# Kernel tuning notes

Hardware: AMD Instinct MI355X
Metric: run time of the kernel (lower is better)

## Reference

```python
import jax, jax.numpy as jnp
import numpy as np

# --- static config (from init_kwargs) ---
B = 256        # num graphs
NPG = 128      # nodes per graph
EPG = 512      # edges per graph
DIN = 128      # dim_node
D = 256        # dim_hidden
RATIO = 0.5    # causal_ratio
N_RES = int(RATIO * EPG)
BN_EPS = 1e-5


def setup_inputs() -> dict:
    key = jax.random.key(0)
    ks = jax.random.split(key, 24)
    N = B * NPG
    x = jax.random.normal(ks[0], (N, DIN), jnp.float32)
    # edges confined within each graph, contiguous per graph (graph-sorted)
    src = jax.random.randint(ks[1], (B, EPG), 0, NPG)
    dst = jax.random.randint(ks[2], (B, EPG), 0, NPG)
    off = (jnp.arange(B, dtype=jnp.int32) * NPG)[:, None]
    edge_index = jnp.stack([(src + off).reshape(-1), (dst + off).reshape(-1)], 0).astype(jnp.int32)
    batch = jnp.repeat(jnp.arange(B, dtype=jnp.int32), NPG)

    s = 0.05
    def rn(k, shape):
        return jax.random.normal(k, shape, jnp.float32) * s
    p = dict(
        x=x, edge_index=edge_index, batch=batch,
        vemb=rn(ks[3], (1, D)),
        # conv1 GIN mlp: Linear(DIN,2D) -> BN -> ReLU -> Linear(2D,D)
        W1a=rn(ks[4], (DIN, 2 * D)), b1a=jnp.zeros((2 * D,)),
        g1a=jnp.ones((2 * D,)), be1a=jnp.zeros((2 * D,)),
        W1b=rn(ks[5], (2 * D, D)), b1b=jnp.zeros((D,)),
        g1=jnp.ones((D,)), be1=jnp.zeros((D,)),          # outer batch_norm1
        # conv2 GIN mlp
        W2a=rn(ks[6], (D, 2 * D)), b2a=jnp.zeros((2 * D,)),
        g2a=jnp.ones((2 * D,)), be2a=jnp.zeros((2 * D,)),
        W2b=rn(ks[7], (2 * D, D)), b2b=jnp.zeros((D,)),
        g2=jnp.ones((D,)), be2=jnp.zeros((D,)),          # outer batch_norm2
        # edge scorer: Linear(2D, 1)
        Wl=rn(ks[8], (2 * D, 1)), bl=jnp.zeros((1,)),
    )
    return p


def _bn(h, g, b):
    mu = h.mean(0)
    var = jnp.mean((h - mu) ** 2, 0)
    return (h - mu) * jax.lax.rsqrt(var + BN_EPS) * g + b


def reference(x, edge_index, batch, vemb,
              W1a, b1a, g1a, be1a, W1b, b1b, g1, be1,
              W2a, b2a, g2a, be2a, W2b, b2b, g2, be2,
              Wl, bl):
    N = x.shape[0]
    row, col = edge_index[0], edge_index[1]

    def gin(h, Wa, ba, ga, bta, Wb, bb):
        # GINConv, eps=0: mlp(h + sum_{j->i} h_j), aggregate src feats at dst
        agg = jax.ops.segment_sum(h[row], col, num_segments=N)
        z = (h + agg) @ Wa + ba
        z = jax.nn.relu(_bn(z, ga, bta))
        return z @ Wb + bb

    # layer 1: conv1 -> bn -> relu (dropout_rate = 0)
    post = jax.nn.relu(_bn(gin(x, W1a, b1a, g1a, be1a, W1b, b1b), g1, be1))
    # virtual node gather (embedding of index 0, one per graph)
    vfeat = jnp.broadcast_to(vemb[0], (B, D))
    post = post + vfeat[batch]
    # layer 2 (last): conv2 -> bn, no relu
    xn = _bn(gin(post, W2a, b2a, g2a, be2a, W2b, b2b), g2, be2)

    # edge scoring
    erep = jnp.concatenate([xn[row], xn[col]], axis=-1)          # [E, 2D]
    pred = (erep @ Wl + bl.astype(erep.dtype)).reshape(-1)       # [E]

    # per-graph top-k split (equal EPG edges per graph)
    pw = pred.reshape(B, EPG)
    order = jnp.argsort(-pw, axis=1)
    idx_r, idx_d = order[:, :N_RES], order[:, N_RES:]
    causal_w = jnp.take_along_axis(pw, idx_r, 1).reshape(-1)
    conf_w = -jnp.take_along_axis(pw, idx_d, 1).reshape(-1)
    ei = edge_index.reshape(2, B, EPG)
    causal_ei = jnp.take_along_axis(ei, jnp.broadcast_to(idx_r[None], (2, B, N_RES)), axis=2).reshape(2, -1)
    conf_ei = jnp.take_along_axis(ei, jnp.broadcast_to(idx_d[None], (2, B, EPG - N_RES)), axis=2).reshape(2, -1)
    return (causal_ei, causal_w, conf_ei, conf_w, pred)
```

## Files before the change

kernel.cpp:

```cpp
#include <hip/hip_runtime.h>

#define BGR   256
#define NPG   128
#define EPG   512
#define DIN   128
#define DD    256
#define DD2   512
#define NTOT  (BGR * NPG)
#define ETOT  (BGR * EPG)
#define NRES  (EPG / 2)
#define NCHUNK 256
#define MP    136

#define OFF_CEI  0
#define OFF_CW   (2 * BGR * NRES)
#define OFF_FEI  (OFF_CW + BGR * NRES)
#define OFF_FW   (OFF_FEI + 2 * BGR * NRES)
#define OFF_PRED (OFF_FW + BGR * NRES)

typedef unsigned short ushortt;
typedef __attribute__((ext_vector_type(4))) unsigned short us4;
typedef __attribute__((ext_vector_type(8))) unsigned short us8;
typedef __attribute__((ext_vector_type(8))) short short8;
typedef __attribute__((ext_vector_type(4))) float f32x4;

__device__ __forceinline__ ushortt f2bf(float f) {
    unsigned int u = __float_as_uint(f);
    unsigned int r = (u + 0x7fffu + ((u >> 16) & 1u)) >> 16;
    return (ushortt)r;
}
__device__ __forceinline__ float bf2f(ushortt u) {
    return __uint_as_float(((unsigned int)u) << 16);
}

__device__ __forceinline__ void g2lds16(const void* g, void* l) {
    __builtin_amdgcn_global_load_lds(
        (const __attribute__((address_space(1))) unsigned int*)g,
        (__attribute__((address_space(3))) unsigned int*)l, 16, 0, 0);
}

__global__ __launch_bounds__(256) void convert_all(const float* __restrict__ W1a,
                                                   const float* __restrict__ W1b,
                                                   const float* __restrict__ W2a,
                                                   const float* __restrict__ W2b,
                                                   ushortt* __restrict__ Wt1a,
                                                   ushortt* __restrict__ Wt1b,
                                                   ushortt* __restrict__ Wt2a,
                                                   ushortt* __restrict__ Wt2b) {
    const int idx = blockIdx.x * 256 + threadIdx.x;
    if (idx < 65536) {
        const int k = idx >> 9, n = idx & 511;
        Wt1a[n * DIN + k] = f2bf(W1a[idx]);
    } else if (idx < 196608) {
        const int i = idx - 65536;
        const int k = i >> 8, n = i & 255;
        Wt1b[n * DD2 + k] = f2bf(W1b[i]);
    } else if (idx < 327680) {
        const int i = idx - 196608;
        const int k = i >> 9, n = i & 511;
        Wt2a[n * DD + k] = f2bf(W2a[i]);
    } else if (idx < 458752) {
        const int i = idx - 327680;
        const int k = i >> 8, n = i & 255;
        Wt2b[n * DD2 + k] = f2bf(W2b[i]);
    }
}

__global__ __launch_bounds__(256) void build_adj(const int* __restrict__ ei,
                                                 ushortt* __restrict__ Madj) {
    __shared__ int cnt[NPG * NPG];
    const int b = blockIdx.x, t = threadIdx.x;
    for (int i = t; i < NPG * NPG; i += 256) cnt[i] = 0;
    __syncthreads();
    for (int e = t; e < EPG; e += 256) {
        const int src = ei[b * EPG + e] - b * NPG;
        const int dst = ei[ETOT + b * EPG + e] - b * NPG;
        atomicAdd(&cnt[dst * NPG + src], 1);
    }
    __syncthreads();
#pragma unroll
    for (int k = 0; k < 8; ++k) {
        const int i0 = (t + k * 256) * 8;
        us8 o;
#pragma unroll
        for (int e = 0; e < 8; ++e) {
            const int i = i0 + e;
            const int v = cnt[i] + (((i >> 7) == (i & 127)) ? 1 : 0);
            o[e] = f2bf((float)v);
        }
        *(us8*)&Madj[(size_t)b * NPG * NPG + i0] = o;
    }
}

__global__ __launch_bounds__(256) void agg1_mm(const float* __restrict__ x,
                                               const ushortt* __restrict__ Madj,
                                               ushortt* __restrict__ s1) {
    __shared__ ushortt Ms[NPG * MP];
    __shared__ ushortt XT[DIN * MP];
    const int b = blockIdx.x, t = threadIdx.x;
    const int wave = t >> 6, lane = t & 63;
    const int qd = lane >> 4, r = lane & 15;
    const ushortt* Mg = Madj + (size_t)b * NPG * NPG;
#pragma unroll
    for (int k = 0; k < 8; ++k) {
        const int ch = t + k * 256;
        const int m = ch >> 4, sc = (ch & 15) * 8;
        *(us8*)&Ms[m * MP + sc] = *(const us8*)&Mg[m * NPG + sc];
    }
#pragma unroll 4
    for (int it = 0; it < 64; ++it) {
        const int s = it * 2 + (t >> 7);
        const int c = t & 127;
        XT[c * MP + s] = f2bf(x[(size_t)(b * NPG + s) * DIN + c]);
    }
    __syncthreads();
    const int wm = (wave >> 1) * 64, wn = (wave & 1) * 64;
    f32x4 acc[4][4] = {};
#pragma unroll
    for (int ks = 0; ks < 4; ++ks) {
        const int k0 = ks * 32 + qd * 8;
        short8 af[4], bfr[4];
#pragma unroll
        for (int i = 0; i < 4; ++i)
            af[i] = *(const short8*)&Ms[(wm + i * 16 + r) * MP + k0];
#pragma unroll
        for (int j = 0; j < 4; ++j)
            bfr[j] = *(const short8*)&XT[(wn + j * 16 + r) * MP + k0];
#pragma unroll
        for (int i = 0; i < 4; ++i)
#pragma unroll
            for (int j = 0; j < 4; ++j)
                acc[i][j] = __builtin_amdgcn_mfma_f32_16x16x32_bf16(af[i], bfr[j], acc[i][j], 0, 0, 0);
    }
    __syncthreads();
    ushortt* Cs = Ms;
#pragma unroll
    for (int j = 0; j < 4; ++j) {
        const int coll = wn + j * 16 + r;
#pragma unroll
        for (int i = 0; i < 4; ++i)
#pragma unroll
            for (int tt = 0; tt < 4; ++tt)
                Cs[(wm + i * 16 + qd * 4 + tt) * DIN + coll] = f2bf(acc[i][j][tt]);
    }
    __syncthreads();
#pragma unroll
    for (int k = 0; k < 8; ++k) {
        const int ch = t + k * 256;
        const int row = ch >> 4, colc = (ch & 15) * 8;
        *(us8*)&s1[(size_t)(b * NPG + row) * DIN + colc] = *(const us8*)&Cs[row * DIN + colc];
    }
}

__global__ __launch_bounds__(256) void agg2_mm(const ushortt* __restrict__ h,
                                               const float* __restrict__ scale,
                                               const float* __restrict__ shift,
                                               const float* __restrict__ vemb,
                                               const ushortt* __restrict__ Madj,
                                               ushortt* __restrict__ s2) {
    __shared__ ushortt Ms[NPG * MP];
    __shared__ ushortt PT[NPG * MP];
    const int nb = blockIdx.x, b = blockIdx.y, t = threadIdx.x;
    const int wave = t >> 6, lane = t & 63;
    const int qd = lane >> 4, r = lane & 15;
    const ushortt* Mg = Madj + (size_t)b * NPG * NPG;
#pragma unroll
    for (int k = 0; k < 8; ++k) {
        const int ch = t + k * 256;
        const int m = ch >> 4, sc = (ch & 15) * 8;
        *(us8*)&Ms[m * MP + sc] = *(const us8*)&Mg[m * NPG + sc];
    }
    const int cl = t & 127;
    const int c = nb * 128 + cl;
    const float scv = scale[c], shv = shift[c], vev = vemb[c];
#pragma unroll 4
    for (int it = 0; it < 64; ++it) {
        const int s = it * 2 + (t >> 7);
        float v = fmaf(bf2f(h[(size_t)(b * NPG + s) * DD + c]), scv, shv);
        PT[cl * MP + s] = f2bf(fmaxf(v, 0.0f) + vev);
    }
    __syncthreads();
    const int wm = (wave >> 1) * 64, wn = (wave & 1) * 64;
    f32x4 acc[4][4] = {};
#pragma unroll
    for (int ks = 0; ks < 4; ++ks) {
        const int k0 = ks * 32 + qd * 8;
        short8 af[4], bfr[4];
#pragma unroll
        for (int i = 0; i < 4; ++i)
            af[i] = *(const short8*)&Ms[(wm + i * 16 + r) * MP + k0];
#pragma unroll
        for (int j = 0; j < 4; ++j)
            bfr[j] = *(const short8*)&PT[(wn + j * 16 + r) * MP + k0];
#pragma unroll
        for (int i = 0; i < 4; ++i)
#pragma unroll
            for (int j = 0; j < 4; ++j)
                acc[i][j] = __builtin_amdgcn_mfma_f32_16x16x32_bf16(af[i], bfr[j], acc[i][j], 0, 0, 0);
    }
    __syncthreads();
    ushortt* Cs = Ms;
#pragma unroll
    for (int j = 0; j < 4; ++j) {
        const int coll = wn + j * 16 + r;
#pragma unroll
        for (int i = 0; i < 4; ++i)
#pragma unroll
            for (int tt = 0; tt < 4; ++tt)
                Cs[(wm + i * 16 + qd * 4 + tt) * 128 + coll] = f2bf(acc[i][j][tt]);
    }
    __syncthreads();
#pragma unroll
    for (int k = 0; k < 8; ++k) {
        const int ch = t + k * 256;
        const int row = ch >> 4, colc = (ch & 15) * 8;
        *(us8*)&s2[(size_t)(b * NPG + row) * DD + nb * 128 + colc] =
            *(const us8*)&Cs[row * 128 + colc];
    }
}

#define BM 128
#define BN 128
#define BK 32
__global__ __launch_bounds__(256) void gemm_mfma(const ushortt* __restrict__ A,
                                                 const ushortt* __restrict__ Wt,
                                                 const float* __restrict__ bias,
                                                 ushortt* __restrict__ C,
                                                 float* __restrict__ psum,
                                                 float* __restrict__ psumsq,
                                                 int M, int N, int K) {
    __shared__ ushortt As[BM * BK];
    __shared__ ushortt Bs[BN * BK];
    __shared__ ushortt Cs[BM * BN];
    __shared__ float redS[2][BN];
    __shared__ float redQ[2][BN];
    const int tid  = threadIdx.x;
    const int wave = tid >> 6;
    const int lane = tid & 63;
    const int qd = lane >> 4;
    const int r  = lane & 15;
    const int wm = (wave >> 1) * 64;
    const int wn = (wave & 1) * 64;
    const int m0 = blockIdx.y * BM;
    const int n0 = blockIdx.x * BN;

    f32x4 acc[4][4] = {};

    for (int k0 = 0; k0 < K; k0 += BK) {
#pragma unroll
        for (int s = 0; s < 2; ++s) {
            const int o   = wave * 128 + s * 64 + lane;
            const int row = o >> 2;
            const int cg  = o & 3;
            g2lds16(A  + (size_t)(m0 + row) * K + k0 + cg * 8,
                    &As[(size_t)(wave * 128 + s * 64) * 8]);
            g2lds16(Wt + (size_t)(n0 + row) * K + k0 + cg * 8,
                    &Bs[(size_t)(wave * 128 + s * 64) * 8]);
        }
        __syncthreads();
        short8 af[4], bfr[4];
#pragma unroll
        for (int i = 0; i < 4; ++i)
            af[i] = *(const short8*)&As[(wm + i * 16 + r) * BK + qd * 8];
#pragma unroll
        for (int j = 0; j < 4; ++j)
            bfr[j] = *(const short8*)&Bs[(wn + j * 16 + r) * BK + qd * 8];
#pragma unroll
        for (int i = 0; i < 4; ++i)
#pragma unroll
            for (int j = 0; j < 4; ++j)
                acc[i][j] = __builtin_amdgcn_mfma_f32_16x16x32_bf16(af[i], bfr[j], acc[i][j], 0, 0, 0);
        __syncthreads();
    }

#pragma unroll
    for (int j = 0; j < 4; ++j) {
        const int coll = wn + j * 16 + r;
        const float bv = bias[n0 + coll];
        float s = 0.0f, q = 0.0f;
#pragma unroll
        for (int i = 0; i < 4; ++i) {
#pragma unroll
            for (int t = 0; t < 4; ++t) {
                const float v = acc[i][j][t] + bv;
                Cs[(wm + i * 16 + qd * 4 + t) * BN + coll] = f2bf(v);
                s += v;
                q = fmaf(v, v, q);
            }
        }
        s += __shfl_xor(s, 16); s += __shfl_xor(s, 32);
        q += __shfl_xor(q, 16); q += __shfl_xor(q, 32);
        if (qd == 0) {
            redS[wave >> 1][coll] = s;
            redQ[wave >> 1][coll] = q;
        }
    }
    __syncthreads();
    if (tid < BN) {
        psum[(size_t)blockIdx.y * N + n0 + tid]   = redS[0][tid] + redS[1][tid];
        psumsq[(size_t)blockIdx.y * N + n0 + tid] = redQ[0][tid] + redQ[1][tid];
    }
#pragma unroll
    for (int s8 = 0; s8 < 8; ++s8) {
        const int c    = tid + 256 * s8;
        const int row  = c >> 4;
        const int colc = (c & 15) * 8;
        const us8 v = *(const us8*)&Cs[row * BN + colc];
        *(us8*)&C[(size_t)(m0 + row) * N + n0 + colc] = v;
    }
}

__global__ __launch_bounds__(256) void bn_finalize(const float* __restrict__ psum,
                                                   const float* __restrict__ psumsq,
                                                   const float* __restrict__ g,
                                                   const float* __restrict__ be,
                                                   int ncols,
                                                   float* __restrict__ scale,
                                                   float* __restrict__ shift) {
    const int c = blockIdx.x * 256 + threadIdx.x;
    double s = 0.0, s2 = 0.0;
    for (int k = 0; k < NCHUNK; ++k) {
        s += (double)psum[(size_t)k * ncols + c];
        s2 += (double)psumsq[(size_t)k * ncols + c];
    }
    const double mean = s / (double)NTOT;
    const double var = s2 / (double)NTOT - mean * mean;
    const double rs = 1.0 / sqrt(var + 1e-5);
    const float sc = (float)((double)g[c] * rs);
    scale[c] = sc;
    shift[c] = (float)((double)be[c] - mean * (double)sc);
}

__global__ __launch_bounds__(256) void bn_apply_vec(const ushortt* __restrict__ z,
                                                    const float* __restrict__ scale,
                                                    const float* __restrict__ shift,
                                                    ushortt* __restrict__ outp,
                                                    int ncolmask) {
    const size_t gi = (size_t)blockIdx.x * 256 + threadIdx.x;
    const size_t base = gi * 8;
    const int c0 = (int)(base & (size_t)ncolmask);
    const us8 z8 = *(const us8*)&z[base];
    us8 o;
#pragma unroll
    for (int e = 0; e < 8; ++e) {
        float v = fmaf(bf2f(z8[e]), scale[c0 + e], shift[c0 + e]);
        v = fmaxf(v, 0.0f);
        o[e] = f2bf(v);
    }
    *(us8*)&outp[base] = o;
}

__global__ __launch_bounds__(256) void node_dots_bn(const ushortt* __restrict__ h2,
                                                    const float* __restrict__ scale,
                                                    const float* __restrict__ shift,
                                                    const float* __restrict__ Wl,
                                                    float* __restrict__ pa,
                                                    float* __restrict__ pb) {
    const int wave = threadIdx.x >> 6;
    const int lane = threadIdx.x & 63;
    const int node = blockIdx.x * 4 + wave;
    const us4 z4 = *(const us4*)&h2[(size_t)node * DD + lane * 4];
    const float4 sc = *(const float4*)&scale[lane * 4];
    const float4 sh = *(const float4*)&shift[lane * 4];
    const float4 w0 = *(const float4*)&Wl[lane * 4];
    const float4 w1 = *(const float4*)&Wl[DD + lane * 4];
    const float x0 = fmaf(bf2f(z4.x), sc.x, sh.x);
    const float x1 = fmaf(bf2f(z4.y), sc.y, sh.y);
    const float x2 = fmaf(bf2f(z4.z), sc.z, sh.z);
    const float x3 = fmaf(bf2f(z4.w), sc.w, sh.w);
    float sa = x0 * w0.x + x1 * w0.y + x2 * w0.z + x3 * w0.w;
    float sb = x0 * w1.x + x1 * w1.y + x2 * w1.z + x3 * w1.w;
#pragma unroll
    for (int off = 32; off >= 1; off >>= 1) {
        sa += __shfl_down(sa, off);
        sb += __shfl_down(sb, off);
    }
    if (lane == 0) {
        pa[node] = sa;
        pb[node] = sb;
    }
}

__global__ __launch_bounds__(EPG) void sort_write(const float* __restrict__ pa,
                                                  const float* __restrict__ pb,
                                                  const float* __restrict__ bl,
                                                  const int* __restrict__ ei,
                                                  float* __restrict__ out) {
    __shared__ float pw[EPG];
    __shared__ int ord[EPG];
    const int b = blockIdx.x;
    const int t = threadIdx.x;
    const int rg = ei[b * EPG + t];
    const int cg = ei[ETOT + b * EPG + t];
    const float v = pa[rg] + pb[cg] + bl[0];
    pw[t] = v;
    out[OFF_PRED + b * EPG + t] = v;
    __syncthreads();
    int rank = 0;
#pragma unroll 8
    for (int k = 0; k < EPG; ++k) {
        const float u = pw[k];
        rank += (u > v) || (u == v && k < t);
    }
    ord[rank] = t;
    __syncthreads();
    const int j = ord[t];
    const float wv = pw[j];
    const float e0 = (float)ei[b * EPG + j];
    const float e1 = (float)ei[ETOT + b * EPG + j];
    if (t < NRES) {
        out[OFF_CEI + b * NRES + t] = e0;
        out[OFF_CEI + BGR * NRES + b * NRES + t] = e1;
        out[OFF_CW + b * NRES + t] = wv;
    } else {
        const int p = t - NRES;
        out[OFF_FEI + b * NRES + p] = e0;
        out[OFF_FEI + BGR * NRES + b * NRES + p] = e1;
        out[OFF_FW + b * NRES + p] = -wv;
    }
}

extern "C" void kernel_launch(void* const* d_in, const int* in_sizes, int n_in,
                              void* d_out, int out_size, void* d_ws, size_t ws_size,
                              hipStream_t stream) {
    (void)in_sizes; (void)n_in; (void)out_size; (void)ws_size;
    const float* x    = (const float*)d_in[0];
    const int*   ei   = (const int*)d_in[1];
    const float* vemb = (const float*)d_in[3];
    const float* W1a  = (const float*)d_in[4];
    const float* b1a  = (const float*)d_in[5];
    const float* g1a  = (const float*)d_in[6];
    const float* be1a = (const float*)d_in[7];
    const float* W1b  = (const float*)d_in[8];
    const float* b1b  = (const float*)d_in[9];
    const float* g1   = (const float*)d_in[10];
    const float* be1  = (const float*)d_in[11];
    const float* W2a  = (const float*)d_in[12];
    const float* b2a  = (const float*)d_in[13];
    const float* g2a  = (const float*)d_in[14];
    const float* be2a = (const float*)d_in[15];
    const float* W2b  = (const float*)d_in[16];
    const float* b2b  = (const float*)d_in[17];
    const float* g2   = (const float*)d_in[18];
    const float* be2  = (const float*)d_in[19];
    const float* Wl   = (const float*)d_in[20];
    const float* bl   = (const float*)d_in[21];
    float* out = (float*)d_out;

    char* wp = (char*)d_ws;
    auto alloc = [&](size_t bytes) -> char* {
        char* r = wp;
        wp += (bytes + 255) & ~(size_t)255;
        return r;
    };
    ushortt* zb    = (ushortt*)alloc((size_t)NTOT * 512 * 2);
    ushortt* bufC  = (ushortt*)alloc((size_t)NTOT * 512 * 2);
    ushortt* bufD  = (ushortt*)alloc((size_t)NTOT * 256 * 2);
    ushortt* bufS1 = (ushortt*)alloc((size_t)NTOT * 128 * 2);
    ushortt* Madj  = (ushortt*)alloc((size_t)BGR * NPG * NPG * 2);
    ushortt* Wt1a  = (ushortt*)alloc((size_t)DIN * DD2 * 2);
    ushortt* Wt1b  = (ushortt*)alloc((size_t)DD2 * DD * 2);
    ushortt* Wt2a  = (ushortt*)alloc((size_t)DD * DD2 * 2);
    ushortt* Wt2b  = (ushortt*)alloc((size_t)DD2 * DD * 2);
    float*   psum   = (float*)alloc((size_t)NCHUNK * 512 * 4);
    float*   psumsq = (float*)alloc((size_t)NCHUNK * 512 * 4);
    float*   scale  = (float*)alloc(512 * 4);
    float*   shift  = (float*)alloc(512 * 4);
    float*   pa     = (float*)alloc((size_t)NTOT * 4);
    float*   pb     = (float*)alloc((size_t)NTOT * 4);

    convert_all<<<1792, 256, 0, stream>>>(W1a, W1b, W2a, W2b, Wt1a, Wt1b, Wt2a, Wt2b);

    build_adj<<<BGR, 256, 0, stream>>>(ei, Madj);

    agg1_mm<<<BGR, 256, 0, stream>>>(x, Madj, bufS1);

    gemm_mfma<<<dim3(DD2 / BN, NTOT / BM), 256, 0, stream>>>(bufS1, Wt1a, b1a, zb, psum, psumsq, NTOT, DD2, DIN);
    bn_finalize<<<2, 256, 0, stream>>>(psum, psumsq, g1a, be1a, DD2, scale, shift);
    bn_apply_vec<<<(NTOT * DD2) / 2048, 256, 0, stream>>>(zb, scale, shift, bufC, DD2 - 1);

    gemm_mfma<<<dim3(DD / BN, NTOT / BM), 256, 0, stream>>>(bufC, Wt1b, b1b, zb, psum, psumsq, NTOT, DD, DD2);
    bn_finalize<<<1, 256, 0, stream>>>(psum, psumsq, g1, be1, DD, scale, shift);

    agg2_mm<<<dim3(2, BGR), 256, 0, stream>>>(zb, scale, shift, vemb, Madj, bufD);

    gemm_mfma<<<dim3(DD2 / BN, NTOT / BM), 256, 0, stream>>>(bufD, Wt2a, b2a, zb, psum, psumsq, NTOT, DD2, DD);
    bn_finalize<<<2, 256, 0, stream>>>(psum, psumsq, g2a, be2a, DD2, scale, shift);
    bn_apply_vec<<<(NTOT * DD2) / 2048, 256, 0, stream>>>(zb, scale, shift, bufC, DD2 - 1);

    gemm_mfma<<<dim3(DD / BN, NTOT / BM), 256, 0, stream>>>(bufC, Wt2b, b2b, zb, psum, psumsq, NTOT, DD, DD2);
    bn_finalize<<<1, 256, 0, stream>>>(psum, psumsq, g2, be2, DD, scale, shift);

    node_dots_bn<<<NTOT / 4, 256, 0, stream>>>(zb, scale, shift, Wl, pa, pb);

    sort_write<<<BGR, EPG, 0, stream>>>(pa, pb, bl, ei, out);
}
```

Measured before the change: 344.7 us.

## Fuse BN-apply into GEMM prologue and BN-finalize into consumers, merge prep kernels

Folds the BatchNorm scale/shift and ReLU into the A-tile load of the second GEMM in each GIN MLP, which removes the separate bn_apply pass over the 512-wide intermediate. The BN finalize for the 256-wide outputs moves into agg2_mm and into a new sort_mega kernel, which also absorbs the per-node dot products. Weight conversion and adjacency building are merged into one launch. Together these cut kernel launches and full-tensor round trips, but every consuming block now redundantly reduces the 256 partial-sum chunks in double precision.

```diff
diff --git a/kernel.cpp b/kernel.cpp
--- a/kernel.cpp
+++ b/kernel.cpp
@@ -39,37 +39,39 @@
         (__attribute__((address_space(3))) unsigned int*)l, 16, 0, 0);
 }
 
-__global__ __launch_bounds__(256) void convert_all(const float* __restrict__ W1a,
-                                                   const float* __restrict__ W1b,
-                                                   const float* __restrict__ W2a,
-                                                   const float* __restrict__ W2b,
-                                                   ushortt* __restrict__ Wt1a,
-                                                   ushortt* __restrict__ Wt1b,
-                                                   ushortt* __restrict__ Wt2a,
-                                                   ushortt* __restrict__ Wt2b) {
-    const int idx = blockIdx.x * 256 + threadIdx.x;
-    if (idx < 65536) {
-        const int k = idx >> 9, n = idx & 511;
-        Wt1a[n * DIN + k] = f2bf(W1a[idx]);
-    } else if (idx < 196608) {
-        const int i = idx - 65536;
-        const int k = i >> 8, n = i & 255;
-        Wt1b[n * DD2 + k] = f2bf(W1b[i]);
-    } else if (idx < 327680) {
-        const int i = idx - 196608;
-        const int k = i >> 9, n = i & 511;
-        Wt2a[n * DD + k] = f2bf(W2a[i]);
-    } else if (idx < 458752) {
-        const int i = idx - 327680;
-        const int k = i >> 8, n = i & 255;
-        Wt2b[n * DD2 + k] = f2bf(W2b[i]);
-    }
-}
-
-__global__ __launch_bounds__(256) void build_adj(const int* __restrict__ ei,
-                                                 ushortt* __restrict__ Madj) {
+__global__ __launch_bounds__(256) void prep(const float* __restrict__ W1a,
+                                            const float* __restrict__ W1b,
+                                            const float* __restrict__ W2a,
+                                            const float* __restrict__ W2b,
+                                            const int* __restrict__ ei,
+                                            ushortt* __restrict__ Wt1a,
+                                            ushortt* __restrict__ Wt1b,
+                                            ushortt* __restrict__ Wt2a,
+                                            ushortt* __restrict__ Wt2b,
+                                            ushortt* __restrict__ Madj) {
     __shared__ int cnt[NPG * NPG];
-    const int b = blockIdx.x, t = threadIdx.x;
+    const int t = threadIdx.x;
+    if (blockIdx.x < 1792) {
+        const int idx = blockIdx.x * 256 + t;
+        if (idx < 65536) {
+            const int k = idx >> 9, n = idx & 511;
+            Wt1a[n * DIN + k] = f2bf(W1a[idx]);
+        } else if (idx < 196608) {
+            const int i = idx - 65536;
+            const int k = i >> 8, n = i & 255;
+            Wt1b[n * DD2 + k] = f2bf(W1b[i]);
+        } else if (idx < 327680) {
+            const int i = idx - 196608;
+            const int k = i >> 9, n = i & 511;
+            Wt2a[n * DD + k] = f2bf(W2a[i]);
+        } else if (idx < 458752) {
+            const int i = idx - 327680;
+            const int k = i >> 8, n = i & 255;
+            Wt2b[n * DD2 + k] = f2bf(W2b[i]);
+        }
+        return;
+    }
+    const int b = blockIdx.x - 1792;
     for (int i = t; i < NPG * NPG; i += 256) cnt[i] = 0;
     __syncthreads();
     for (int e = t; e < EPG; e += 256) {
@@ -153,13 +155,18 @@
 }
 
 __global__ __launch_bounds__(256) void agg2_mm(const ushortt* __restrict__ h,
-                                               const float* __restrict__ scale,
-                                               const float* __restrict__ shift,
+                                               const float* __restrict__ psum,
+                                               const float* __restrict__ psumsq,
+                                               const float* __restrict__ g,
+                                               const float* __restrict__ be,
                                                const float* __restrict__ vemb,
                                                const ushortt* __restrict__ Madj,
                                                ushortt* __restrict__ s2) {
     __shared__ ushortt Ms[NPG * MP];
     __shared__ ushortt PT[NPG * MP];
+    __shared__ double redS[2][128];
+    __shared__ double redQ[2][128];
+    __shared__ float scs[128], shs[128];
     const int nb = blockIdx.x, b = blockIdx.y, t = threadIdx.x;
     const int wave = t >> 6, lane = t & 63;
     const int qd = lane >> 4, r = lane & 15;
@@ -170,9 +177,34 @@
         const int m = ch >> 4, sc = (ch & 15) * 8;
         *(us8*)&Ms[m * MP + sc] = *(const us8*)&Mg[m * NPG + sc];
     }
+    {
+        const int cl = t & 127, half = t >> 7;
+        const int c = nb * 128 + cl;
+        double s = 0.0, q = 0.0;
+#pragma unroll 4
+        for (int k = half * 128; k < half * 128 + 128; ++k) {
+            s += (double)psum[(size_t)k * DD + c];
+            q += (double)psumsq[(size_t)k * DD + c];
+        }
+        redS[half][cl] = s;
+        redQ[half][cl] = q;
+    }
+    __syncthreads();
+    if (t < 128) {
+        const int c = nb * 128 + t;
+        const double s = redS[0][t] + redS[1][t];
+        const double q = redQ[0][t] + redQ[1][t];
+        const double mean = s / (double)NTOT;
+        const double var = q / (double)NTOT - mean * mean;
+        const double rs = 1.0 / sqrt(var + 1e-5);
+        const float sc = (float)((double)g[c] * rs);
+        scs[t] = sc;
+        shs[t] = (float)((double)be[c] - mean * (double)sc);
+    }
+    __syncthreads();
     const int cl = t & 127;
     const int c = nb * 128 + cl;
-    const float scv = scale[c], shv = shift[c], vev = vemb[c];
+    const float scv = scs[cl], shv = shs[cl], vev = vemb[c];
 #pragma unroll 4
     for (int it = 0; it < 64; ++it) {
         const int s = it * 2 + (t >> 7);
@@ -310,6 +342,122 @@
     }
 }
 
+__global__ __launch_bounds__(256) void gemm_mfma_bn(const ushortt* __restrict__ A,
+                                                    const ushortt* __restrict__ Wt,
+                                                    const float* __restrict__ scale,
+                                                    const float* __restrict__ shift,
+                                                    const float* __restrict__ bias,
+                                                    ushortt* __restrict__ C,
+                                                    float* __restrict__ psum,
+                                                    float* __restrict__ psumsq,
+                                                    int M, int N, int K) {
+    __shared__ ushortt As[BM * BK];
+    __shared__ ushortt Bs[BN * BK];
+    __shared__ ushortt Cs[BM * BN];
+    __shared__ float redS[2][BN];
+    __shared__ float redQ[2][BN];
+    __shared__ float scs[DD2], shs[DD2];
+    const int tid  = threadIdx.x;
+    const int wave = tid >> 6;
+    const int lane = tid & 63;
+    const int qd = lane >> 4;
+    const int r  = lane & 15;
+    const int wm = (wave >> 1) * 64;
+    const int wn = (wave & 1) * 64;
+    const int m0 = blockIdx.y * BM;
+    const int n0 = blockIdx.x * BN;
+
+    for (int i = tid; i < K; i += 256) {
+        scs[i] = scale[i];
+        shs[i] = shift[i];
+    }
+    __syncthreads();
+
+    f32x4 acc[4][4] = {};
+
+    for (int k0 = 0; k0 < K; k0 += BK) {
+#pragma unroll
+        for (int s = 0; s < 2; ++s) {
+            const int o   = wave * 128 + s * 64 + lane;
+            const int row = o >> 2;
+            const int cg  = o & 3;
+            g2lds16(Wt + (size_t)(n0 + row) * K + k0 + cg * 8,
+                    &Bs[(size_t)(wave * 128 + s * 64) * 8]);
+        }
+#pragma unroll
+        for (int s = 0; s < 2; ++s) {
+            const int o   = wave * 128 + s * 64 + lane;
+            const int row = o >> 2;
+            const int cg  = o & 3;
+            const us8 a8 = *(const us8*)&A[(size_t)(m0 + row) * K + k0 + cg * 8];
+            const float4 s4a = *(const float4*)&scs[k0 + cg * 8];
+            const float4 s4b = *(const float4*)&scs[k0 + cg * 8 + 4];
+            const float4 h4a = *(const float4*)&shs[k0 + cg * 8];
+            const float4 h4b = *(const float4*)&shs[k0 + cg * 8 + 4];
+            us8 t8;
+            t8[0] = f2bf(fmaxf(fmaf(bf2f(a8[0]), s4a.x, h4a.x), 0.0f));
+            t8[1] = f2bf(fmaxf(fmaf(bf2f(a8[1]), s4a.y, h4a.y), 0.0f));
+            t8[2] = f2bf(fmaxf(fmaf(bf2f(a8[2]), s4a.z, h4a.z), 0.0f));
+            t8[3] = f2bf(fmaxf(fmaf(bf2f(a8[3]), s4a.w, h4a.w), 0.0f));
+            t8[4] = f2bf(fmaxf(fmaf(bf2f(a8[4]), s4b.x, h4b.x), 0.0f));
+            t8[5] = f2bf(fmaxf(fmaf(bf2f(a8[5]), s4b.y, h4b.y), 0.0f));
+            t8[6] = f2bf(fmaxf(fmaf(bf2f(a8[6]), s4b.z, h4b.z), 0.0f));
+            t8[7] = f2bf(fmaxf(fmaf(bf2f(a8[7]), s4b.w, h4b.w), 0.0f));
+            *(us8*)&As[row * BK + cg * 8] = t8;
+        }
+        __syncthreads();
+        short8 af[4], bfr[4];
+#pragma unroll
+        for (int i = 0; i < 4; ++i)
+            af[i] = *(const short8*)&As[(wm + i * 16 + r) * BK + qd * 8];
+#pragma unroll
+        for (int j = 0; j < 4; ++j)
+            bfr[j] = *(const short8*)&Bs[(wn + j * 16 + r) * BK + qd * 8];
+#pragma unroll
+        for (int i = 0; i < 4; ++i)
+#pragma unroll
+            for (int j = 0; j < 4; ++j)
+                acc[i][j] = __builtin_amdgcn_mfma_f32_16x16x32_bf16(af[i], bfr[j], acc[i][j], 0, 0, 0);
+        __syncthreads();
+    }
+
+#pragma unroll
+    for (int j = 0; j < 4; ++j) {
+        const int coll = wn + j * 16 + r;
+        const float bv = bias[n0 + coll];
+        float s = 0.0f, q = 0.0f;
+#pragma unroll
+        for (int i = 0; i < 4; ++i) {
+#pragma unroll
+            for (int t = 0; t < 4; ++t) {
+                const float v = acc[i][j][t] + bv;
+                Cs[(wm + i * 16 + qd * 4 + t) * BN + coll] = f2bf(v);
+                s += v;
+                q = fmaf(v, v, q);
+            }
+        }
+        s += __shfl_xor(s, 16); s += __shfl_xor(s, 32);
+        q += __shfl_xor(q, 16); q += __shfl_xor(q, 32);
+        if (qd == 0) {
+            redS[wave >> 1][coll] = s;
+            redQ[wave >> 1][coll] = q;
+        }
+    }
+    __syncthreads();
+    if (tid < BN) {
+        psum[(size_t)blockIdx.y * N + n0 + tid]   = redS[0][tid] + redS[1][tid];
+        psumsq[(size_t)blockIdx.y * N + n0 + tid] = redQ[0][tid] + redQ[1][tid];
+    }
+#pragma unroll
+    for (int s8 = 0; s8 < 8; ++s8) {
+        const int c    = tid + 256 * s8;
+        const int row  = c >> 4;
+        const int colc = (c & 15) * 8;
+        const us8 v = *(const us8*)&Cs[row * BN + colc];
+        *(us8*)&C[(size_t)(m0 + row) * N + n0 + colc] = v;
+    }
+}
+
 __global__ __launch_bounds__(256) void bn_finalize(const float* __restrict__ psum,
                                                    const float* __restrict__ psumsq,
                                                    const float* __restrict__ g,
@@ -331,68 +479,71 @@
     shift[c] = (float)((double)be[c] - mean * (double)sc);
 }
 
-__global__ __launch_bounds__(256) void bn_apply_vec(const ushortt* __restrict__ z,
-                                                    const float* __restrict__ scale,
-                                                    const float* __restrict__ shift,
-                                                    ushortt* __restrict__ outp,
-                                                    int ncolmask) {
-    const size_t gi = (size_t)blockIdx.x * 256 + threadIdx.x;
-    const size_t base = gi * 8;
-    const int c0 = (int)(base & (size_t)ncolmask);
-    const us8 z8 = *(const us8*)&z[base];
-    us8 o;
-#pragma unroll
-    for (int e = 0; e < 8; ++e) {
-        float v = fmaf(bf2f(z8[e]), scale[c0 + e], shift[c0 + e]);
-        v = fmaxf(v, 0.0f);
-        o[e] = f2bf(v);
-    }
-    *(us8*)&outp[base] = o;
-}
-
-__global__ __launch_bounds__(256) void node_dots_bn(const ushortt* __restrict__ h2,
-                                                    const float* __restrict__ scale,
-                                                    const float* __restrict__ shift,
-                                                    const float* __restrict__ Wl,
-                                                    float* __restrict__ pa,
-                                                    float* __restrict__ pb) {
-    const int wave = threadIdx.x >> 6;
-    const int lane = threadIdx.x & 63;
-    const int node = blockIdx.x * 4 + wave;
-    const us4 z4 = *(const us4*)&h2[(size_t)node * DD + lane * 4];
-    const float4 sc = *(const float4*)&scale[lane * 4];
-    const float4 sh = *(const float4*)&shift[lane * 4];
-    const float4 w0 = *(const float4*)&Wl[lane * 4];
-    const float4 w1 = *(const float4*)&Wl[DD + lane * 4];
-    const float x0 = fmaf(bf2f(z4.x), sc.x, sh.x);
-    const float x1 = fmaf(bf2f(z4.y), sc.y, sh.y);
-    const float x2 = fmaf(bf2f(z4.z), sc.z, sh.z);
-    const float x3 = fmaf(bf2f(z4.w), sc.w, sh.w);
-    float sa = x0 * w0.x + x1 * w0.y + x2 * w0.z + x3 * w0.w;
-    float sb = x0 * w1.x + x1 * w1.y + x2 * w1.z + x3 * w1.w;
-#pragma unroll
-    for (int off = 32; off >= 1; off >>= 1) {
-        sa += __shfl_down(sa, off);
-        sb += __shfl_down(sb, off);
-    }
-    if (lane == 0) {
-        pa[node] = sa;
-        pb[node] = sb;
-    }
-}
-
-__global__ __launch_bounds__(EPG) void sort_write(const float* __restrict__ pa,
-                                                  const float* __restrict__ pb,
-                                                  const float* __restrict__ bl,
-                                                  const int* __restrict__ ei,
-                                                  float* __restrict__ out) {
+__global__ __launch_bounds__(EPG) void sort_mega(const ushortt* __restrict__ h2,
+                                                 const float* __restrict__ psum,
+                                                 const float* __restrict__ psumsq,
+                                                 const float* __restrict__ g,
+                                                 const float* __restrict__ be,
+                                                 const float* __restrict__ Wl,
+                                                 const float* __restrict__ bl,
+                                                 const int* __restrict__ ei,
+                                                 float* __restrict__ out) {
+    __shared__ double redS[2][DD];
+    __shared__ double redQ[2][DD];
+    __shared__ float scs[DD], shs[DD];
+    __shared__ float pa[NPG], pb[NPG];
     __shared__ float pw[EPG];
     __shared__ int ord[EPG];
-    const int b = blockIdx.x;
-    const int t = threadIdx.x;
-    const int rg = ei[b * EPG + t];
-    const int cg = ei[ETOT + b * EPG + t];
-    const float v = pa[rg] + pb[cg] + bl[0];
+    const int b = blockIdx.x, t = threadIdx.x;
+    {
+        const int c = t & 255, half = t >> 8;
+        double s = 0.0, q = 0.0;
+#pragma unroll 4
+        for (int k = half * 128; k < half * 128 + 128; ++k) {
+            s += (double)psum[(size_t)k * DD + c];
+            q += (double)psumsq[(size_t)k * DD + c];
+        }
+        redS[half][c] = s;
+        redQ[half][c] = q;
+    }
+    __syncthreads();
+    if (t < DD) {
+        const double s = redS[0][t] + redS[1][t];
+        const double q = redQ[0][t] + redQ[1][t];
+        const double mean = s / (double)NTOT;
+        const double var = q / (double)NTOT - mean * mean;
+        const double rs = 1.0 / sqrt(var + 1e-5);
+        const float sc = (float)((double)g[t] * rs);
+        scs[t] = sc;
+        shs[t] = (float)((double)be[t] - mean * (double)sc);
+    }
+    __syncthreads();
+    {
+        const int wave = t >> 6, lane = t & 63;
+        const float4 w0 = *(const float4*)&Wl[lane * 4];
+        const float4 w1 = *(const float4*)&Wl[DD + lane * 4];
+        const float4 sc4 = *(const float4*)&scs[lane * 4];
+        const float4 sh4 = *(const float4*)&shs[lane * 4];
+        for (int n = wave; n < NPG; n += 8) {
+            const us4 z4 = *(const us4*)&h2[(size_t)(b * NPG + n) * DD + lane * 4];
+            const float x0 = fmaf(bf2f(z4.x), sc4.x, sh4.x);
+            const float x1 = fmaf(bf2f(z4.y), sc4.y, sh4.y);
+            const float x2 = fmaf(bf2f(z4.z), sc4.z, sh4.z);
+            const float x3 = fmaf(bf2f(z4.w), sc4.w, sh4.w);
+            float sa = x0 * w0.x + x1 * w0.y + x2 * w0.z + x3 * w0.w;
+            float sb = x0 * w1.x + x1 * w1.y + x2 * w1.z + x3 * w1.w;
+#pragma unroll
+            for (int off = 32; off >= 1; off >>= 1) {
+                sa += __shfl_down(sa, off);
+                sb += __shfl_down(sb, off);
+            }
+            if (lane == 0) { pa[n] = sa; pb[n] = sb; }
+        }
+    }
+    __syncthreads();
+    const int rl = ei[b * EPG + t] - b * NPG;
+    const int cl = ei[ETOT + b * EPG + t] - b * NPG;
+    const float v = pa[rl] + pb[cl] + bl[0];
     pw[t] = v;
     out[OFF_PRED + b * EPG + t] = v;
     __syncthreads();
@@ -454,7 +605,7 @@
         return r;
     };
     ushortt* zb    = (ushortt*)alloc((size_t)NTOT * 512 * 2);
-    ushortt* bufC  = (ushortt*)alloc((size_t)NTOT * 512 * 2);
+    ushortt* bufC  = (ushortt*)alloc((size_t)NTOT * 256 * 2);
     ushortt* bufD  = (ushortt*)alloc((size_t)NTOT * 256 * 2);
     ushortt* bufS1 = (ushortt*)alloc((size_t)NTOT * 128 * 2);
     ushortt* Madj  = (ushortt*)alloc((size_t)BGR * NPG * NPG * 2);
@@ -466,32 +617,23 @@
     float*   psumsq = (float*)alloc((size_t)NCHUNK * 512 * 4);
     float*   scale  = (float*)alloc(512 * 4);
     float*   shift  = (float*)alloc(512 * 4);
-    float*   pa     = (float*)alloc((size_t)NTOT * 4);
-    float*   pb     = (float*)alloc((size_t)NTOT * 4);
-
-    convert_all<<<1792, 256, 0, stream>>>(W1a, W1b, W2a, W2b, Wt1a, Wt1b, Wt2a, Wt2b);
-
-    build_adj<<<BGR, 256, 0, stream>>>(ei, Madj);
+
+    prep<<<2048, 256, 0, stream>>>(W1a, W1b, W2a, W2b, ei,
+                                   Wt1a, Wt1b, Wt2a, Wt2b, Madj);
 
     agg1_mm<<<BGR, 256, 0, stream>>>(x, Madj, bufS1);
 
     gemm_mfma<<<dim3(DD2 / BN, NTOT / BM), 256, 0, stream>>>(bufS1, Wt1a, b1a, zb, psum, psumsq, NTOT, DD2, DIN);
     bn_finalize<<<2, 256, 0, stream>>>(psum, psumsq, g1a, be1a, DD2, scale, shift);
-    bn_apply_vec<<<(NTOT * DD2) / 2048, 256, 0, stream>>>(zb, scale, shift, bufC, DD2 - 1);
-
-    gemm_mfma<<<dim3(DD / BN, NTOT / BM), 256, 0, stream>>>(bufC, Wt1b, b1b, zb, psum, psumsq, NTOT, DD, DD2);
-    bn_finalize<<<1, 256, 0, stream>>>(psum, psumsq, g1, be1, DD, scale, shift);
-
-    agg2_mm<<<dim3(2, BGR), 256, 0, stream>>>(zb, scale, shift, vemb, Madj, bufD);
+
+    gemm_mfma_bn<<<dim3(DD / BN, NTOT / BM), 256, 0, stream>>>(zb, Wt1b, scale, shift, b1b, bufC, psum, psumsq, NTOT, DD, DD2);
+
+    agg2_mm<<<dim3(2, BGR), 256, 0, stream>>>(bufC, psum, psumsq, g1, be1, vemb, Madj, bufD);
 
     gemm_mfma<<<dim3(DD2 / BN, NTOT / BM), 256, 0, stream>>>(bufD, Wt2a, b2a, zb, psum, psumsq, NTOT, DD2, DD);
     bn_finalize<<<2, 256, 0, stream>>>(psum, psumsq, g2a, be2a, DD2, scale, shift);
-    bn_apply_vec<<<(NTOT * DD2) / 2048, 256, 0, stream>>>(zb, scale, shift, bufC, DD2 - 1);
-
-    gemm_mfma<<<dim3(DD / BN, NTOT / BM), 256, 0, stream>>>(bufC, Wt2b, b2b, zb, psum, psumsq, NTOT, DD, DD2);
-    bn_finalize<<<1, 256, 0, stream>>>(psum, psumsq, g2, be2, DD, scale, shift);
-
-    node_dots_bn<<<NTOT / 4, 256, 0, stream>>>(zb, scale, shift, Wl, pa, pb);
-
-    sort_write<<<BGR, EPG, 0, stream>>>(pa, pb, bl, ei, out);
-}
+
+    gemm_mfma_bn<<<dim3(DD / BN, NTOT / BM), 256, 0, stream>>>(zb, Wt2b, scale, shift, b2b, bufC, psum, psumsq, NTOT, DD, DD2);
+
+    sort_mega<<<BGR, EPG, 0, stream>>>(bufC, psum, psumsq, g2, be2, Wl, bl, ei, out);
+}
```

New measurement: 311.6 us. -9.6%, faster.
